# Kernel tuning notes

Measured on AMD Instinct MI355X. Metric: run time of the kernel, lower is better.

## Reference

```python
import jax, jax.numpy as jnp
import numpy as np

N_EMBD = 1024
N_HEAD = 16
HEAD_SIZE = N_EMBD // N_HEAD  # 64


def rotate_half(x):
    x1, x2 = x[..., : x.shape[-1] // 2], x[..., x.shape[-1] // 2 :]
    return jnp.concatenate([-x2, x1], axis=-1)


def rope_cos_sin(T, head_size, dtype):
    inv_freq = 1.0 / (10000.0 ** (jnp.arange(0, head_size, 2, dtype=jnp.float32) / head_size))
    t = jnp.arange(T, dtype=jnp.float32)
    freqs = jnp.outer(t, inv_freq)  # (T, D/2)
    emb = jnp.concatenate([freqs, freqs], axis=-1)  # (T, D)
    return jnp.cos(emb).astype(dtype), jnp.sin(emb).astype(dtype)


def setup_inputs() -> dict:
    key = jax.random.key(0)
    k1, k2, k3, k4 = jax.random.split(key, 4)
    B, T, C = 4, 4096, N_EMBD
    scale = 1.0 / np.sqrt(C)
    return {
        "x": jax.random.normal(k1, (B, T, C), dtype=jnp.float32),
        "sigma0": jnp.zeros((B, N_HEAD, HEAD_SIZE, HEAD_SIZE), dtype=jnp.float32),
        "w_qkv": jax.random.normal(k2, (3 * C, C), dtype=jnp.float32) * scale,
        "w_proj": jax.random.normal(k3, (C, C), dtype=jnp.float32) * scale,
        "eta": jnp.ones((1,), dtype=jnp.float32) * 0.1,
    }


def reference(x, sigma0, w_qkv, w_proj, eta):
    B, T, C = x.shape
    H, D = N_HEAD, HEAD_SIZE
    qkv = x @ w_qkv.T  # (B,T,3C)
    q, k, v = jnp.split(qkv, 3, axis=-1)
    # (B,T,C) -> (B,H,T,D)
    q = q.reshape(B, T, H, D).transpose(0, 2, 1, 3)
    k = k.reshape(B, T, H, D).transpose(0, 2, 1, 3)
    v = v.reshape(B, T, H, D).transpose(0, 2, 1, 3)
    cos, sin = rope_cos_sin(T, D, x.dtype)  # (T,D) broadcast over (B,H,T,D)
    q = q * cos + rotate_half(q) * sin
    k = k * cos + rotate_half(k) * sin
    q = jax.nn.relu(q)
    k = jax.nn.relu(k)
    # sequential Hebbian fast-weight scan over time
    q_t = q.transpose(2, 0, 1, 3)  # (T,B,H,D)
    k_t = k.transpose(2, 0, 1, 3)
    v_t = v.transpose(2, 0, 1, 3)
    eta_s = eta[0]

    def step(sigma, qkv_step):
        qt, kt, vt = qkv_step  # each (B,H,D)
        out_t = jnp.einsum("bhd,bhde->bhe", qt, sigma)  # read BEFORE update
        sigma = sigma + eta_s * jnp.einsum("bhd,bhe->bhde", kt, vt)
        return sigma, out_t

    sigma_final, outs = jax.lax.scan(step, sigma0, (q_t, k_t, v_t))
    # outs: (T,B,H,D) -> (B,T,C)
    out = outs.transpose(1, 0, 2, 3).reshape(B, T, C)
    out = out @ w_proj.T
    return out, sigma_final
```

## Files before the change

### kernel.cpp

```cpp
#include <hip/hip_runtime.h>
#include <hip/hip_bf16.h>
#include <cstdint>
#include <cstddef>

#define B_   4
#define T_   4096
#define C_   1024
#define H_   16
#define NC_  64
#define M_   (B_*T_)
#define N3_  (3*C_)

typedef __attribute__((ext_vector_type(4))) float  f32x4;
typedef __attribute__((ext_vector_type(8))) __bf16 bf16x8;
typedef __attribute__((ext_vector_type(4))) __bf16 bf16x4;
typedef __attribute__((ext_vector_type(8))) unsigned short u16x8;

__device__ __forceinline__ void glds16(void* lds, const void* g) {
  __builtin_amdgcn_global_load_lds((const __attribute__((address_space(1))) void*)g,
                                   (__attribute__((address_space(3))) void*)lds,
                                   16, 0, 0);
}

__global__ __launch_bounds__(256) void cvt_f32_bf16(const float* __restrict__ in,
                                                    __bf16* __restrict__ out, int n4) {
  int i = blockIdx.x * 256 + threadIdx.x;
  if (i >= n4) return;
  float4 v = reinterpret_cast<const float4*>(in)[i];
  bf16x4 o;
  o[0] = (__bf16)v.x; o[1] = (__bf16)v.y; o[2] = (__bf16)v.z; o[3] = (__bf16)v.w;
  reinterpret_cast<bf16x4*>(out)[i] = o;
}

__global__ __launch_bounds__(256) void rope_tab(float2* __restrict__ tab) {
  int gid = blockIdx.x * 256 + threadIdx.x;
  int t = gid >> 5, dp = gid & 31;
  float invf = exp2f(-(float)dp * (13.287712379549449f / 32.0f));
  float ang = (float)t * invf;
  float s, c;
  sincosf(ang, &s, &c);
  tab[gid] = make_float2(c, s);
}

template<int FUSE>
__global__ __launch_bounds__(256) void gemm_bt(const __bf16* __restrict__ A,
                                               const __bf16* __restrict__ Bt,
                                               void* __restrict__ Cout,
                                               const float2* __restrict__ tab,
                                               int M, int N, int K) {
  __shared__ __bf16 sA[128 * 32];
  __shared__ __bf16 sB[128 * 32];
  const int tid  = threadIdx.x;
  const int lane = tid & 63;
  const int wave = tid >> 6;
  const int wr = wave >> 1, wc = wave & 1;
  const int bm = blockIdx.y, bn = blockIdx.x;

  const int srow = wave * 32 + (lane >> 2);
  const int scol = (lane & 3) * 8;
  const __bf16* Ag = A  + (size_t)(bm * 128 + srow) * K + scol;
  const __bf16* Bg = Bt + (size_t)(bn * 128 + srow) * K + scol;
  __bf16* lA0 = sA + wave * 1024 + lane * 8;
  __bf16* lA1 = lA0 + 512;
  __bf16* lB0 = sB + wave * 1024 + lane * 8;
  __bf16* lB1 = lB0 + 512;

  f32x4 acc[4][4];
#pragma unroll
  for (int i = 0; i < 4; i++)
#pragma unroll
    for (int j = 0; j < 4; j++) acc[i][j] = (f32x4)0.0f;

  const int fr = lane & 15;
  const int kb = (lane >> 4) * 8;

  for (int kt = 0; kt < K; kt += 32) {
    __syncthreads();
    glds16(lA0, Ag + kt);
    glds16(lA1, Ag + (size_t)16 * K + kt);
    glds16(lB0, Bg + kt);
    glds16(lB1, Bg + (size_t)16 * K + kt);
    __syncthreads();
    bf16x8 af[4], bfr[4];
#pragma unroll
    for (int i = 0; i < 4; i++)
      af[i] = *(const bf16x8*)(sA + (wr * 64 + i * 16 + fr) * 32 + kb);
#pragma unroll
    for (int j = 0; j < 4; j++)
      bfr[j] = *(const bf16x8*)(sB + (wc * 64 + j * 16 + fr) * 32 + kb);
#pragma unroll
    for (int i = 0; i < 4; i++)
#pragma unroll
      for (int j = 0; j < 4; j++)
        acc[i][j] = __builtin_amdgcn_mfma_f32_16x16x32_bf16(af[i], bfr[j], acc[i][j], 0, 0, 0);
  }

  const int rg = (lane >> 4) * 4;
  if (FUSE == 1 && bn < 16) {
#pragma unroll
    for (int i = 0; i < 4; i++) {
#pragma unroll
      for (int r = 0; r < 4; r++) {
        size_t row = (size_t)bm * 128 + wr * 64 + i * 16 + rg + r;
        int t = (int)(row & (T_ - 1));
#pragma unroll
        for (int j = 0; j < 2; j++) {
          int dp = j * 16 + fr;
          float2 cs = tab[t * 32 + dp];
          float x1 = acc[i][j][r], x2 = acc[i][j + 2][r];
          float o1 = fmaxf(x1 * cs.x - x2 * cs.y, 0.0f);
          float o2 = fmaxf(x2 * cs.x + x1 * cs.y, 0.0f);
          size_t col = (size_t)bn * 128 + wc * 64 + j * 16 + fr;
          ((__bf16*)Cout)[row * N + col]      = (__bf16)o1;
          ((__bf16*)Cout)[row * N + col + 32] = (__bf16)o2;
        }
      }
    }
  } else {
#pragma unroll
    for (int i = 0; i < 4; i++) {
#pragma unroll
      for (int j = 0; j < 4; j++) {
        size_t row = (size_t)bm * 128 + wr * 64 + i * 16 + rg;
        size_t col = (size_t)bn * 128 + wc * 64 + j * 16 + fr;
#pragma unroll
        for (int r = 0; r < 4; r++) {
          if (FUSE == 2) ((float*)Cout)[(row + r) * N + col]  = acc[i][j][r];
          else           ((__bf16*)Cout)[(row + r) * N + col] = (__bf16)acc[i][j][r];
        }
      }
    }
  }
}

#define LDW 72
__global__ __launch_bounds__(256) void chunk_kv(const __bf16* __restrict__ qkv,
                                                __bf16* __restrict__ G) {
  __shared__ __bf16 Kt[64 * LDW];
  __shared__ __bf16 Vt[64 * LDW];
  const int bid = blockIdx.x;
  const int c = bid & (NC_ - 1);
  const int bh = bid >> 6;
  const int h = bh & (H_ - 1);
  const int b = bh >> 4;
  const int tid = threadIdx.x;
  const size_t row0 = (size_t)b * T_ + c * 64;
  const int kcol = C_ + h * 64;
  const int vcol = 2 * C_ + h * 64;
#pragma unroll
  for (int it = 0; it < 2; ++it) {
    int task = tid + it * 256;
    int t = task >> 3;
    int d0 = (task & 7) * 8;
    const size_t rb = (row0 + t) * N3_;
    u16x8 kv = *(const u16x8*)(qkv + rb + kcol + d0);
    u16x8 vv = *(const u16x8*)(qkv + rb + vcol + d0);
#pragma unroll
    for (int j = 0; j < 8; j++) {
      ((unsigned short*)Kt)[(d0 + j) * LDW + t] = kv[j];
      ((unsigned short*)Vt)[(d0 + j) * LDW + t] = vv[j];
    }
  }
  __syncthreads();
  const int lane = tid & 63, wave = tid >> 6;
  const int gr = (wave >> 1) * 32, gc = (wave & 1) * 32;
  const int fr = lane & 15, kb = (lane >> 4) * 8;
  f32x4 acc[2][2];
#pragma unroll
  for (int i = 0; i < 2; i++)
#pragma unroll
    for (int j = 0; j < 2; j++) acc[i][j] = (f32x4)0.0f;
#pragma unroll
  for (int kk = 0; kk < 2; ++kk) {
    bf16x8 af[2], bfr[2];
#pragma unroll
    for (int i = 0; i < 2; i++)
      af[i] = *(const bf16x8*)(Kt + (gr + i * 16 + fr) * LDW + kk * 32 + kb);
#pragma unroll
    for (int j = 0; j < 2; j++)
      bfr[j] = *(const bf16x8*)(Vt + (gc + j * 16 + fr) * LDW + kk * 32 + kb);
#pragma unroll
    for (int i = 0; i < 2; i++)
#pragma unroll
      for (int j = 0; j < 2; j++)
        acc[i][j] = __builtin_amdgcn_mfma_f32_16x16x32_bf16(af[i], bfr[j], acc[i][j], 0, 0, 0);
  }
  const int rg = (lane >> 4) * 4;
  __bf16* Gb = G + (size_t)bid * 4096;
#pragma unroll
  for (int i = 0; i < 2; i++)
#pragma unroll
    for (int j = 0; j < 2; j++)
#pragma unroll
      for (int r = 0; r < 4; r++)
        Gb[(gr + i * 16 + rg + r) * 64 + gc + j * 16 + fr] = (__bf16)acc[i][j][r];
}

__global__ __launch_bounds__(256) void prefix_scan(const __bf16* __restrict__ G,
                                                   const float* __restrict__ sigma0,
                                                   __bf16* __restrict__ S,
                                                   float* __restrict__ sigma_out,
                                                   const float* __restrict__ eta) {
  const int blk = blockIdx.x;
  const int bh = blk >> 2;
  const int dq = blk & 3;
  const int tid = threadIdx.x;
  const int d = dq * 16 + (tid >> 4);
  const int e0 = (tid & 15) * 4;
  const float eta_s = eta[0];
  const size_t base_de = (size_t)d * 64 + e0;
  float acc[4], s0[4];
#pragma unroll
  for (int j = 0; j < 4; j++) {
    acc[j] = 0.0f;
    s0[j] = sigma0[(size_t)bh * 4096 + base_de + j];
  }
  for (int c = 0; c < NC_; ++c) {
    const size_t off = ((size_t)bh * NC_ + c) * 4096 + base_de;
    bf16x4 sv;
#pragma unroll
    for (int j = 0; j < 4; j++) sv[j] = (__bf16)(s0[j] + eta_s * acc[j]);
    *(bf16x4*)(S + off) = sv;
    bf16x4 g = *(const bf16x4*)(G + off);
#pragma unroll
    for (int j = 0; j < 4; j++) acc[j] += (float)g[j];
  }
  float4 v;
  v.x = s0[0] + eta_s * acc[0];
  v.y = s0[1] + eta_s * acc[1];
  v.z = s0[2] + eta_s * acc[2];
  v.w = s0[3] + eta_s * acc[3];
  *reinterpret_cast<float4*>(sigma_out + (size_t)bh * 4096 + base_de) = v;
}

__global__ __launch_bounds__(256) void chunk_out(const __bf16* __restrict__ qkv,
                                                 const __bf16* __restrict__ S,
                                                 __bf16* __restrict__ outp,
                                                 const float* __restrict__ eta) {
  __shared__ __bf16 Qs[64 * LDW];
  __shared__ __bf16 Ks[64 * LDW];
  __shared__ __bf16 Vt[64 * LDW];
  __shared__ __bf16 St[64 * LDW];
  __shared__ __bf16 Ps[64 * LDW];
  const int bid = blockIdx.x;
  const int c = bid & 63, bh = bid >> 6, h = bh & 15, b = bh >> 4;
  const int tid = threadIdx.x;
  const size_t row0 = (size_t)b * T_ + c * 64;
  const float eta_s = eta[0];
#pragma unroll
  for (int it = 0; it < 2; ++it) {
    int task = tid + it * 256;
    int t = task >> 3, d0 = (task & 7) * 8;
    const size_t rb = (row0 + t) * N3_;
    *(u16x8*)(Qs + t * LDW + d0) = *(const u16x8*)(qkv + rb + h * 64 + d0);
    *(u16x8*)(Ks + t * LDW + d0) = *(const u16x8*)(qkv + rb + C_ + h * 64 + d0);
    u16x8 vv = *(const u16x8*)(qkv + rb + 2 * C_ + h * 64 + d0);
    u16x8 sv = *(const u16x8*)(S + (size_t)bid * 4096 + t * 64 + d0);
#pragma unroll
    for (int j = 0; j < 8; j++) {
      ((unsigned short*)Vt)[(d0 + j) * LDW + t] = vv[j];
      ((unsigned short*)St)[(d0 + j) * LDW + t] = sv[j];
    }
  }
  __syncthreads();
  const int lane = tid & 63, wave = tid >> 6;
  const int qr = (wave >> 1) * 32, qc = (wave & 1) * 32;
  const int fr = lane & 15, kb = (lane >> 4) * 8, rg = (lane >> 4) * 4;
  {
    f32x4 pacc[2][2];
#pragma unroll
    for (int i = 0; i < 2; i++)
#pragma unroll
      for (int j = 0; j < 2; j++) pacc[i][j] = (f32x4)0.0f;
#pragma unroll
    for (int kk = 0; kk < 2; ++kk) {
      bf16x8 af[2], bfr[2];
#pragma unroll
      for (int i = 0; i < 2; i++)
        af[i] = *(const bf16x8*)(Qs + (qr + i * 16 + fr) * LDW + kk * 32 + kb);
#pragma unroll
      for (int j = 0; j < 2; j++)
        bfr[j] = *(const bf16x8*)(Ks + (qc + j * 16 + fr) * LDW + kk * 32 + kb);
#pragma unroll
      for (int i = 0; i < 2; i++)
#pragma unroll
        for (int j = 0; j < 2; j++)
          pacc[i][j] = __builtin_amdgcn_mfma_f32_16x16x32_bf16(af[i], bfr[j], pacc[i][j], 0, 0, 0);
    }
#pragma unroll
    for (int i = 0; i < 2; i++)
#pragma unroll
      for (int j = 0; j < 2; j++)
#pragma unroll
        for (int r = 0; r < 4; r++) {
          int trow = qr + i * 16 + rg + r;
          int scol = qc + j * 16 + fr;
          float v = (scol < trow) ? eta_s * pacc[i][j][r] : 0.0f;
          Ps[trow * LDW + scol] = (__bf16)v;
        }
  }
  __syncthreads();
  {
    f32x4 oacc[2][2];
#pragma unroll
    for (int i = 0; i < 2; i++)
#pragma unroll
      for (int j = 0; j < 2; j++) oacc[i][j] = (f32x4)0.0f;
#pragma unroll
    for (int kk = 0; kk < 2; ++kk) {
      bf16x8 pa[2], vb[2], qa[2], sb[2];
#pragma unroll
      for (int i = 0; i < 2; i++) {
        pa[i] = *(const bf16x8*)(Ps + (qr + i * 16 + fr) * LDW + kk * 32 + kb);
        qa[i] = *(const bf16x8*)(Qs + (qr + i * 16 + fr) * LDW + kk * 32 + kb);
      }
#pragma unroll
      for (int j = 0; j < 2; j++) {
        vb[j] = *(const bf16x8*)(Vt + (qc + j * 16 + fr) * LDW + kk * 32 + kb);
        sb[j] = *(const bf16x8*)(St + (qc + j * 16 + fr) * LDW + kk * 32 + kb);
      }
#pragma unroll
      for (int i = 0; i < 2; i++)
#pragma unroll
        for (int j = 0; j < 2; j++) {
          oacc[i][j] = __builtin_amdgcn_mfma_f32_16x16x32_bf16(pa[i], vb[j], oacc[i][j], 0, 0, 0);
          oacc[i][j] = __builtin_amdgcn_mfma_f32_16x16x32_bf16(qa[i], sb[j], oacc[i][j], 0, 0, 0);
        }
    }
#pragma unroll
    for (int i = 0; i < 2; i++)
#pragma unroll
      for (int j = 0; j < 2; j++)
#pragma unroll
        for (int r = 0; r < 4; r++) {
          size_t row = row0 + qr + i * 16 + rg + r;
          int col = h * 64 + qc + j * 16 + fr;
          outp[row * C_ + col] = (__bf16)oacc[i][j][r];
        }
  }
}

extern "C" void kernel_launch(void* const* d_in, const int* in_sizes, int n_in,
                              void* d_out, int out_size, void* d_ws, size_t ws_size,
                              hipStream_t stream) {
  const float* x      = (const float*)d_in[0];
  const float* sigma0 = (const float*)d_in[1];
  const float* w_qkv  = (const float*)d_in[2];
  const float* w_proj = (const float*)d_in[3];
  const float* eta    = (const float*)d_in[4];
  float* out       = (float*)d_out;
  float* sigma_out = out + (size_t)M_ * C_;

  char* ws = (char*)d_ws;
  __bf16* xbf     = (__bf16*)(ws);
  __bf16* wqkvbf  = (__bf16*)(ws + 33554432);
  __bf16* wprojbf = (__bf16*)(ws + 39845888);
  __bf16* qkvbf   = (__bf16*)(ws + 41943040);
  __bf16* Gws     = (__bf16*)(ws + 142606336);
  __bf16* Sws     = (__bf16*)(ws + 176160768);
  float2* tab     = (float2*)(ws + 176160768);

  rope_tab<<<512, 256, 0, stream>>>(tab);
  cvt_f32_bf16<<<16384, 256, 0, stream>>>(x, xbf, 4194304);
  cvt_f32_bf16<<<3072, 256, 0, stream>>>(w_qkv, wqkvbf, 786432);
  cvt_f32_bf16<<<1024, 256, 0, stream>>>(w_proj, wprojbf, 262144);
  gemm_bt<1><<<dim3(24, 128), 256, 0, stream>>>(xbf, wqkvbf, (void*)qkvbf, tab, M_, N3_, C_);
  chunk_kv<<<4096, 256, 0, stream>>>(qkvbf, Gws);
  prefix_scan<<<256, 256, 0, stream>>>(Gws, sigma0, Sws, sigma_out, eta);
  chunk_out<<<4096, 256, 0, stream>>>(qkvbf, Sws, xbf, eta);
  gemm_bt<2><<<dim3(8, 128), 256, 0, stream>>>(xbf, wprojbf, (void*)out, nullptr, M_, C_, C_);
}
```

Measured before the change: 296.6 us.

## Replace QKV GEMM with triple-buffered 256x128 tile pipelined kernel

Result: faster. 280.4 us (-5.5%).

```diff
diff --git a/kernel.cpp b/kernel.cpp
--- a/kernel.cpp
+++ b/kernel.cpp
@@ -10,6 +10,7 @@
 #define NC_  64
 #define M_   (B_*T_)
 #define N3_  (3*C_)
+#define G1_NT 16
 
 typedef __attribute__((ext_vector_type(4))) float  f32x4;
 typedef __attribute__((ext_vector_type(8))) __bf16 bf16x8;
@@ -21,6 +22,7 @@
                                    (__attribute__((address_space(3))) void*)lds,
                                    16, 0, 0);
 }
+#define MFMA_BF16 __builtin_amdgcn_mfma_f32_16x16x32_bf16
 
 __global__ __launch_bounds__(256) void cvt_f32_bf16(const float* __restrict__ in,
                                                     __bf16* __restrict__ out, int n4) {
@@ -42,12 +44,150 @@
   tab[gid] = make_float2(c, s);
 }
 
-template<int FUSE>
-__global__ __launch_bounds__(256) void gemm_bt(const __bf16* __restrict__ A,
-                                               const __bf16* __restrict__ Bt,
-                                               void* __restrict__ Cout,
-                                               const float2* __restrict__ tab,
-                                               int M, int N, int K) {
+__global__ __launch_bounds__(512) void gemm1_pipe(const __bf16* __restrict__ A,
+                                                  const __bf16* __restrict__ Bt,
+                                                  __bf16* __restrict__ Cout,
+                                                  const float2* __restrict__ tab) {
+  __shared__ __bf16 sA[3][256 * 64];
+  __shared__ __bf16 sB[3][128 * 64];
+  const int tid  = threadIdx.x;
+  const int lane = tid & 63;
+  const int wave = tid >> 6;
+  const int wm = wave >> 1, wn = wave & 1;
+  const int bm = blockIdx.y, bn = blockIdx.x;
+  const int fr = lane & 15, kq = lane >> 4;
+  const int fr7 = fr & 7;
+  const int K = C_;
+
+  const int r_loc = tid >> 3;
+  const int sslot = (tid & 7) ^ (r_loc & 7);
+  const __bf16* Ag = A  + (size_t)(bm * 256 + r_loc) * K + sslot * 8;
+  const __bf16* Bg = Bt + (size_t)(bn * 128 + r_loc) * K + sslot * 8;
+
+  f32x4 acc[4][4];
+#pragma unroll
+  for (int i = 0; i < 4; i++)
+#pragma unroll
+    for (int j = 0; j < 4; j++) acc[i][j] = (f32x4)0.0f;
+
+#pragma unroll
+  for (int t = 0; t < 2; ++t) {
+#pragma unroll
+    for (int q = 0; q < 4; ++q)
+      glds16((char*)sA[t] + q * 8192 + tid * 16, Ag + (size_t)q * 64 * K + t * 64);
+#pragma unroll
+    for (int q = 0; q < 2; ++q)
+      glds16((char*)sB[t] + q * 8192 + tid * 16, Bg + (size_t)q * 64 * K + t * 64);
+  }
+  asm volatile("s_waitcnt vmcnt(6)" ::: "memory");
+  __builtin_amdgcn_sched_barrier(0);
+  __builtin_amdgcn_s_barrier();
+
+  bf16x8 af[4][2], bf01[2][2], bf23[2][2];
+  for (int t = 0; t < G1_NT; ++t) {
+    const int buf  = t % 3;
+    const int nbuf = (t + 2) % 3;
+    const bool dostage = (t + 2 < G1_NT);
+    const int kb2 = (t + 2) * 64;
+    const __bf16* Ab = (const __bf16*)sA[buf];
+    const __bf16* Bb = (const __bf16*)sB[buf];
+
+    if (dostage) {
+      glds16((char*)sA[nbuf] +     0 + tid * 16, Ag + (size_t)0 * 64 * K + kb2);
+      glds16((char*)sA[nbuf] +  8192 + tid * 16, Ag + (size_t)1 * 64 * K + kb2);
+      glds16((char*)sA[nbuf] + 16384 + tid * 16, Ag + (size_t)2 * 64 * K + kb2);
+    }
+#pragma unroll
+    for (int i = 0; i < 4; ++i)
+#pragma unroll
+      for (int kk = 0; kk < 2; ++kk)
+        af[i][kk] = *(const bf16x8*)((const char*)Ab + (wm * 64 + i * 16 + fr) * 128 +
+                                     (((kk << 2) | kq) ^ fr7) * 16);
+#pragma unroll
+    for (int j = 0; j < 2; ++j)
+#pragma unroll
+      for (int kk = 0; kk < 2; ++kk)
+        bf01[j][kk] = *(const bf16x8*)((const char*)Bb + (wn * 64 + j * 16 + fr) * 128 +
+                                       (((kk << 2) | kq) ^ fr7) * 16);
+    __builtin_amdgcn_s_barrier();
+    __builtin_amdgcn_s_setprio(1);
+#pragma unroll
+    for (int i = 0; i < 4; ++i)
+#pragma unroll
+      for (int j = 0; j < 2; ++j) {
+        acc[i][j] = MFMA_BF16(af[i][0], bf01[j][0], acc[i][j], 0, 0, 0);
+        acc[i][j] = MFMA_BF16(af[i][1], bf01[j][1], acc[i][j], 0, 0, 0);
+      }
+    __builtin_amdgcn_s_setprio(0);
+    __builtin_amdgcn_s_barrier();
+
+    if (dostage) {
+      glds16((char*)sA[nbuf] + 24576 + tid * 16, Ag + (size_t)3 * 64 * K + kb2);
+      glds16((char*)sB[nbuf] +     0 + tid * 16, Bg + (size_t)0 * 64 * K + kb2);
+      glds16((char*)sB[nbuf] +  8192 + tid * 16, Bg + (size_t)1 * 64 * K + kb2);
+    }
+#pragma unroll
+    for (int j = 0; j < 2; ++j)
+#pragma unroll
+      for (int kk = 0; kk < 2; ++kk)
+        bf23[j][kk] = *(const bf16x8*)((const char*)Bb + (wn * 64 + (j + 2) * 16 + fr) * 128 +
+                                       (((kk << 2) | kq) ^ fr7) * 16);
+    __builtin_amdgcn_s_barrier();
+    __builtin_amdgcn_s_setprio(1);
+#pragma unroll
+    for (int i = 0; i < 4; ++i)
+#pragma unroll
+      for (int j = 0; j < 2; ++j) {
+        acc[i][j + 2] = MFMA_BF16(af[i][0], bf23[j][0], acc[i][j + 2], 0, 0, 0);
+        acc[i][j + 2] = MFMA_BF16(af[i][1], bf23[j][1], acc[i][j + 2], 0, 0, 0);
+      }
+    __builtin_amdgcn_s_setprio(0);
+    if (t < G1_NT - 1) {
+      if (dostage) asm volatile("s_waitcnt vmcnt(6)" ::: "memory");
+      else         asm volatile("s_waitcnt vmcnt(0)" ::: "memory");
+      __builtin_amdgcn_sched_barrier(0);
+    }
+    __builtin_amdgcn_s_barrier();
+  }
+
+  const int rg4 = kq * 4;
+  if (bn < 16) {
+#pragma unroll
+    for (int i = 0; i < 4; ++i)
+#pragma unroll
+      for (int r = 0; r < 4; ++r) {
+        size_t row = (size_t)bm * 256 + wm * 64 + i * 16 + rg4 + r;
+        int tt = (int)(row & (T_ - 1));
+#pragma unroll
+        for (int j = 0; j < 2; ++j) {
+          int dp = j * 16 + fr;
+          float2 cs = tab[tt * 32 + dp];
+          float x1 = acc[i][j][r], x2 = acc[i][j + 2][r];
+          float o1 = fmaxf(x1 * cs.x - x2 * cs.y, 0.0f);
+          float o2 = fmaxf(x2 * cs.x + x1 * cs.y, 0.0f);
+          size_t col = (size_t)bn * 128 + wn * 64 + j * 16 + fr;
+          Cout[row * N3_ + col]      = (__bf16)o1;
+          Cout[row * N3_ + col + 32] = (__bf16)o2;
+        }
+      }
+  } else {
+#pragma unroll
+    for (int i = 0; i < 4; ++i)
+#pragma unroll
+      for (int j = 0; j < 4; ++j) {
+        size_t row = (size_t)bm * 256 + wm * 64 + i * 16 + rg4;
+        size_t col = (size_t)bn * 128 + wn * 64 + j * 16 + fr;
+#pragma unroll
+        for (int r = 0; r < 4; ++r)
+          Cout[(row + r) * N3_ + col] = (__bf16)acc[i][j][r];
+      }
+  }
+}
+
+__global__ __launch_bounds__(256) void gemm_bt_f32(const __bf16* __restrict__ A,
+                                                   const __bf16* __restrict__ Bt,
+                                                   float* __restrict__ Cout,
+                                                   int M, int N, int K) {
   __shared__ __bf16 sA[128 * 32];
   __shared__ __bf16 sB[128 * 32];
   const int tid  = threadIdx.x;
@@ -92,45 +232,20 @@
     for (int i = 0; i < 4; i++)
 #pragma unroll
       for (int j = 0; j < 4; j++)
-        acc[i][j] = __builtin_amdgcn_mfma_f32_16x16x32_bf16(af[i], bfr[j], acc[i][j], 0, 0, 0);
+        acc[i][j] = MFMA_BF16(af[i], bfr[j], acc[i][j], 0, 0, 0);
   }
 
   const int rg = (lane >> 4) * 4;
-  if (FUSE == 1 && bn < 16) {
-#pragma unroll
-    for (int i = 0; i < 4; i++) {
-#pragma unroll
-      for (int r = 0; r < 4; r++) {
-        size_t row = (size_t)bm * 128 + wr * 64 + i * 16 + rg + r;
-        int t = (int)(row & (T_ - 1));
-#pragma unroll
-        for (int j = 0; j < 2; j++) {
-          int dp = j * 16 + fr;
-          float2 cs = tab[t * 32 + dp];
-          float x1 = acc[i][j][r], x2 = acc[i][j + 2][r];
-          float o1 = fmaxf(x1 * cs.x - x2 * cs.y, 0.0f);
-          float o2 = fmaxf(x2 * cs.x + x1 * cs.y, 0.0f);
-          size_t col = (size_t)bn * 128 + wc * 64 + j * 16 + fr;
-          ((__bf16*)Cout)[row * N + col]      = (__bf16)o1;
-          ((__bf16*)Cout)[row * N + col + 32] = (__bf16)o2;
-        }
-      }
-    }
-  } else {
-#pragma unroll
-    for (int i = 0; i < 4; i++) {
-#pragma unroll
-      for (int j = 0; j < 4; j++) {
-        size_t row = (size_t)bm * 128 + wr * 64 + i * 16 + rg;
-        size_t col = (size_t)bn * 128 + wc * 64 + j * 16 + fr;
-#pragma unroll
-        for (int r = 0; r < 4; r++) {
-          if (FUSE == 2) ((float*)Cout)[(row + r) * N + col]  = acc[i][j][r];
-          else           ((__bf16*)Cout)[(row + r) * N + col] = (__bf16)acc[i][j][r];
-        }
-      }
-    }
-  }
+#pragma unroll
+  for (int i = 0; i < 4; i++)
+#pragma unroll
+    for (int j = 0; j < 4; j++) {
+      size_t row = (size_t)bm * 128 + wr * 64 + i * 16 + rg;
+      size_t col = (size_t)bn * 128 + wc * 64 + j * 16 + fr;
+#pragma unroll
+      for (int r = 0; r < 4; r++)
+        Cout[(row + r) * N + col] = acc[i][j][r];
+    }
 }
 
 #define LDW 72
@@ -183,7 +298,7 @@
     for (int i = 0; i < 2; i++)
 #pragma unroll
       for (int j = 0; j < 2; j++)
-        acc[i][j] = __builtin_amdgcn_mfma_f32_16x16x32_bf16(af[i], bfr[j], acc[i][j], 0, 0, 0);
+        acc[i][j] = MFMA_BF16(af[i], bfr[j], acc[i][j], 0, 0, 0);
   }
   const int rg = (lane >> 4) * 4;
   __bf16* Gb = G + (size_t)bid * 4096;
@@ -285,7 +400,7 @@
       for (int i = 0; i < 2; i++)
 #pragma unroll
         for (int j = 0; j < 2; j++)
-          pacc[i][j] = __builtin_amdgcn_mfma_f32_16x16x32_bf16(af[i], bfr[j], pacc[i][j], 0, 0, 0);
+          pacc[i][j] = MFMA_BF16(af[i], bfr[j], pacc[i][j], 0, 0, 0);
     }
 #pragma unroll
     for (int i = 0; i < 2; i++)
@@ -323,8 +438,8 @@
       for (int i = 0; i < 2; i++)
 #pragma unroll
         for (int j = 0; j < 2; j++) {
-          oacc[i][j] = __builtin_amdgcn_mfma_f32_16x16x32_bf16(pa[i], vb[j], oacc[i][j], 0, 0, 0);
-          oacc[i][j] = __builtin_amdgcn_mfma_f32_16x16x32_bf16(qa[i], sb[j], oacc[i][j], 0, 0, 0);
+          oacc[i][j] = MFMA_BF16(pa[i], vb[j], oacc[i][j], 0, 0, 0);
+          oacc[i][j] = MFMA_BF16(qa[i], sb[j], oacc[i][j], 0, 0, 0);
         }
     }
 #pragma unroll
@@ -364,9 +479,9 @@
   cvt_f32_bf16<<<16384, 256, 0, stream>>>(x, xbf, 4194304);
   cvt_f32_bf16<<<3072, 256, 0, stream>>>(w_qkv, wqkvbf, 786432);
   cvt_f32_bf16<<<1024, 256, 0, stream>>>(w_proj, wprojbf, 262144);
-  gemm_bt<1><<<dim3(24, 128), 256, 0, stream>>>(xbf, wqkvbf, (void*)qkvbf, tab, M_, N3_, C_);
+  gemm1_pipe<<<dim3(24, 64), 512, 0, stream>>>(xbf, wqkvbf, qkvbf, tab);
   chunk_kv<<<4096, 256, 0, stream>>>(qkvbf, Gws);
   prefix_scan<<<256, 256, 0, stream>>>(Gws, sigma0, Sws, sigma_out, eta);
   chunk_out<<<4096, 256, 0, stream>>>(qkvbf, Sws, xbf, eta);
-  gemm_bt<2><<<dim3(8, 128), 256, 0, stream>>>(xbf, wprojbf, (void*)out, nullptr, M_, C_, C_);
-}
+  gemm_bt_f32<<<dim3(8, 128), 256, 0, stream>>>(xbf, wprojbf, out, M_, C_, C_);
+}
```

## Replace GEMM with 256x256-tile, 4-stage async LDS pipeline and swizzled layout

Applied to the files above, without the earlier changes.

Result: slower. 310.4 us (+4.7%).

```diff
diff --git a/kernel.cpp b/kernel.cpp
--- a/kernel.cpp
+++ b/kernel.cpp
@@ -10,6 +10,7 @@
 #define NC_  64
 #define M_   (B_*T_)
 #define N3_  (3*C_)
+#define NT2  32
 
 typedef __attribute__((ext_vector_type(4))) float  f32x4;
 typedef __attribute__((ext_vector_type(8))) __bf16 bf16x8;
@@ -21,6 +22,7 @@
                                    (__attribute__((address_space(3))) void*)lds,
                                    16, 0, 0);
 }
+#define MFMA_BF16 __builtin_amdgcn_mfma_f32_16x16x32_bf16
 
 __global__ __launch_bounds__(256) void cvt_f32_bf16(const float* __restrict__ in,
                                                     __bf16* __restrict__ out, int n4) {
@@ -43,93 +45,116 @@
 }
 
 template<int FUSE>
-__global__ __launch_bounds__(256) void gemm_bt(const __bf16* __restrict__ A,
-                                               const __bf16* __restrict__ Bt,
-                                               void* __restrict__ Cout,
-                                               const float2* __restrict__ tab,
-                                               int M, int N, int K) {
-  __shared__ __bf16 sA[128 * 32];
-  __shared__ __bf16 sB[128 * 32];
+__global__ __launch_bounds__(512) void gemm_pipe256(const __bf16* __restrict__ A,
+                                                    const __bf16* __restrict__ Bt,
+                                                    void* __restrict__ Cout,
+                                                    const float2* __restrict__ tab,
+                                                    int N) {
+  __shared__ __bf16 sA[4][256 * 32];
+  __shared__ __bf16 sB[4][256 * 32];
   const int tid  = threadIdx.x;
   const int lane = tid & 63;
   const int wave = tid >> 6;
-  const int wr = wave >> 1, wc = wave & 1;
+  const int wm = wave >> 2, wn = wave & 3;
   const int bm = blockIdx.y, bn = blockIdx.x;
-
-  const int srow = wave * 32 + (lane >> 2);
-  const int scol = (lane & 3) * 8;
-  const __bf16* Ag = A  + (size_t)(bm * 128 + srow) * K + scol;
-  const __bf16* Bg = Bt + (size_t)(bn * 128 + srow) * K + scol;
-  __bf16* lA0 = sA + wave * 1024 + lane * 8;
-  __bf16* lA1 = lA0 + 512;
-  __bf16* lB0 = sB + wave * 1024 + lane * 8;
-  __bf16* lB1 = lB0 + 512;
-
-  f32x4 acc[4][4];
-#pragma unroll
-  for (int i = 0; i < 4; i++)
+  const int fr = lane & 15, kq = lane >> 4;
+  const int K = C_;
+
+  const int r_loc = tid >> 2;
+  const int sslot = (tid & 3) ^ (r_loc & 3);
+  const __bf16* Ag = A  + (size_t)(bm * 256 + r_loc) * K + sslot * 8;
+  const __bf16* Bg = Bt + (size_t)(bn * 256 + r_loc) * K + sslot * 8;
+
+  f32x4 acc[8][4];
+#pragma unroll
+  for (int i = 0; i < 8; i++)
 #pragma unroll
     for (int j = 0; j < 4; j++) acc[i][j] = (f32x4)0.0f;
 
-  const int fr = lane & 15;
-  const int kb = (lane >> 4) * 8;
-
-  for (int kt = 0; kt < K; kt += 32) {
-    __syncthreads();
-    glds16(lA0, Ag + kt);
-    glds16(lA1, Ag + (size_t)16 * K + kt);
-    glds16(lB0, Bg + kt);
-    glds16(lB1, Bg + (size_t)16 * K + kt);
-    __syncthreads();
-    bf16x8 af[4], bfr[4];
-#pragma unroll
-    for (int i = 0; i < 4; i++)
-      af[i] = *(const bf16x8*)(sA + (wr * 64 + i * 16 + fr) * 32 + kb);
-#pragma unroll
-    for (int j = 0; j < 4; j++)
-      bfr[j] = *(const bf16x8*)(sB + (wc * 64 + j * 16 + fr) * 32 + kb);
-#pragma unroll
-    for (int i = 0; i < 4; i++)
-#pragma unroll
-      for (int j = 0; j < 4; j++)
-        acc[i][j] = __builtin_amdgcn_mfma_f32_16x16x32_bf16(af[i], bfr[j], acc[i][j], 0, 0, 0);
-  }
-
-  const int rg = (lane >> 4) * 4;
-  if (FUSE == 1 && bn < 16) {
-#pragma unroll
-    for (int i = 0; i < 4; i++) {
-#pragma unroll
-      for (int r = 0; r < 4; r++) {
-        size_t row = (size_t)bm * 128 + wr * 64 + i * 16 + rg + r;
-        int t = (int)(row & (T_ - 1));
-#pragma unroll
-        for (int j = 0; j < 2; j++) {
+#pragma unroll
+  for (int t = 0; t < 3; ++t) {
+    glds16((char*)sA[t] +    0 + tid * 16, Ag + (size_t)0 * 128 * K + t * 32);
+    glds16((char*)sA[t] + 8192 + tid * 16, Ag + (size_t)1 * 128 * K + t * 32);
+    glds16((char*)sB[t] +    0 + tid * 16, Bg + (size_t)0 * 128 * K + t * 32);
+    glds16((char*)sB[t] + 8192 + tid * 16, Bg + (size_t)1 * 128 * K + t * 32);
+  }
+  asm volatile("s_waitcnt vmcnt(8)" ::: "memory");
+  __builtin_amdgcn_sched_barrier(0);
+  __builtin_amdgcn_s_barrier();
+
+  const int swz = (kq ^ (fr & 3)) * 16;
+  bf16x8 af[8], bf4[4];
+  for (int t = 0; t < NT2; ++t) {
+    const int buf  = t & 3;
+    const int nbuf = (t + 3) & 3;
+    const __bf16* Ab = (const __bf16*)sA[buf];
+    const __bf16* Bb = (const __bf16*)sB[buf];
+
+    if (t + 3 < NT2) {
+      const int kb3 = (t + 3) * 32;
+      glds16((char*)sA[nbuf] +    0 + tid * 16, Ag + (size_t)0 * 128 * K + kb3);
+      glds16((char*)sA[nbuf] + 8192 + tid * 16, Ag + (size_t)1 * 128 * K + kb3);
+      glds16((char*)sB[nbuf] +    0 + tid * 16, Bg + (size_t)0 * 128 * K + kb3);
+      glds16((char*)sB[nbuf] + 8192 + tid * 16, Bg + (size_t)1 * 128 * K + kb3);
+    }
+
+#pragma unroll
+    for (int i = 0; i < 8; ++i)
+      af[i] = *(const bf16x8*)((const char*)Ab + (wm * 128 + i * 16 + fr) * 64 + swz);
+#pragma unroll
+    for (int j = 0; j < 4; ++j)
+      bf4[j] = *(const bf16x8*)((const char*)Bb + (wn * 64 + j * 16 + fr) * 64 + swz);
+
+    __builtin_amdgcn_s_setprio(1);
+#pragma unroll
+    for (int i = 0; i < 8; ++i)
+#pragma unroll
+      for (int j = 0; j < 4; ++j)
+        acc[i][j] = MFMA_BF16(af[i], bf4[j], acc[i][j], 0, 0, 0);
+    __builtin_amdgcn_s_setprio(0);
+
+    if (t < NT2 - 1) {
+      if (t < NT2 - 3)       asm volatile("s_waitcnt vmcnt(8)" ::: "memory");
+      else if (t == NT2 - 3) asm volatile("s_waitcnt vmcnt(4)" ::: "memory");
+      else                   asm volatile("s_waitcnt vmcnt(0)" ::: "memory");
+      __builtin_amdgcn_sched_barrier(0);
+      __builtin_amdgcn_s_barrier();
+    }
+  }
+
+  const int rg4 = kq * 4;
+  const int cb = bn * 256 + wn * 64;
+  if (FUSE == 1 && bn < 8) {
+#pragma unroll
+    for (int i = 0; i < 8; ++i)
+#pragma unroll
+      for (int r = 0; r < 4; ++r) {
+        size_t row = (size_t)bm * 256 + wm * 128 + i * 16 + rg4 + r;
+        int tt = (int)(row & (T_ - 1));
+#pragma unroll
+        for (int j = 0; j < 2; ++j) {
           int dp = j * 16 + fr;
-          float2 cs = tab[t * 32 + dp];
+          float2 cs = tab[tt * 32 + dp];
           float x1 = acc[i][j][r], x2 = acc[i][j + 2][r];
           float o1 = fmaxf(x1 * cs.x - x2 * cs.y, 0.0f);
           float o2 = fmaxf(x2 * cs.x + x1 * cs.y, 0.0f);
-          size_t col = (size_t)bn * 128 + wc * 64 + j * 16 + fr;
-          ((__bf16*)Cout)[row * N + col]      = (__bf16)o1;
-          ((__bf16*)Cout)[row * N + col + 32] = (__bf16)o2;
+          ((__bf16*)Cout)[row * N + cb + j * 16 + fr]      = (__bf16)o1;
+          ((__bf16*)Cout)[row * N + cb + j * 16 + fr + 32] = (__bf16)o2;
         }
       }
-    }
   } else {
 #pragma unroll
-    for (int i = 0; i < 4; i++) {
-#pragma unroll
-      for (int j = 0; j < 4; j++) {
-        size_t row = (size_t)bm * 128 + wr * 64 + i * 16 + rg;
-        size_t col = (size_t)bn * 128 + wc * 64 + j * 16 + fr;
-#pragma unroll
-        for (int r = 0; r < 4; r++) {
+    for (int i = 0; i < 8; ++i)
+#pragma unroll
+      for (int j = 0; j < 4; ++j) {
+        size_t row = (size_t)bm * 256 + wm * 128 + i * 16 + rg4;
+        size_t col = (size_t)cb + j * 16 + fr;
+#pragma unroll
+        for (int r = 0; r < 4; ++r) {
           if (FUSE == 2) ((float*)Cout)[(row + r) * N + col]  = acc[i][j][r];
           else           ((__bf16*)Cout)[(row + r) * N + col] = (__bf16)acc[i][j][r];
         }
       }
-    }
   }
 }
 
@@ -183,7 +208,7 @@
     for (int i = 0; i < 2; i++)
 #pragma unroll
       for (int j = 0; j < 2; j++)
-        acc[i][j] = __builtin_amdgcn_mfma_f32_16x16x32_bf16(af[i], bfr[j], acc[i][j], 0, 0, 0);
+        acc[i][j] = MFMA_BF16(af[i], bfr[j], acc[i][j], 0, 0, 0);
   }
   const int rg = (lane >> 4) * 4;
   __bf16* Gb = G + (size_t)bid * 4096;
@@ -285,7 +310,7 @@
       for (int i = 0; i < 2; i++)
 #pragma unroll
         for (int j = 0; j < 2; j++)
-          pacc[i][j] = __builtin_amdgcn_mfma_f32_16x16x32_bf16(af[i], bfr[j], pacc[i][j], 0, 0, 0);
+          pacc[i][j] = MFMA_BF16(af[i], bfr[j], pacc[i][j], 0, 0, 0);
     }
 #pragma unroll
     for (int i = 0; i < 2; i++)
@@ -323,8 +348,8 @@
       for (int i = 0; i < 2; i++)
 #pragma unroll
         for (int j = 0; j < 2; j++) {
-          oacc[i][j] = __builtin_amdgcn_mfma_f32_16x16x32_bf16(pa[i], vb[j], oacc[i][j], 0, 0, 0);
-          oacc[i][j] = __builtin_amdgcn_mfma_f32_16x16x32_bf16(qa[i], sb[j], oacc[i][j], 0, 0, 0);
+          oacc[i][j] = MFMA_BF16(pa[i], vb[j], oacc[i][j], 0, 0, 0);
+          oacc[i][j] = MFMA_BF16(qa[i], sb[j], oacc[i][j], 0, 0, 0);
         }
     }
 #pragma unroll
@@ -364,9 +389,9 @@
   cvt_f32_bf16<<<16384, 256, 0, stream>>>(x, xbf, 4194304);
   cvt_f32_bf16<<<3072, 256, 0, stream>>>(w_qkv, wqkvbf, 786432);
   cvt_f32_bf16<<<1024, 256, 0, stream>>>(w_proj, wprojbf, 262144);
-  gemm_bt<1><<<dim3(24, 128), 256, 0, stream>>>(xbf, wqkvbf, (void*)qkvbf, tab, M_, N3_, C_);
+  gemm_pipe256<1><<<dim3(12, 64), 512, 0, stream>>>(xbf, wqkvbf, (void*)qkvbf, tab, N3_);
   chunk_kv<<<4096, 256, 0, stream>>>(qkvbf, Gws);
   prefix_scan<<<256, 256, 0, stream>>>(Gws, sigma0, Sws, sigma_out, eta);
   chunk_out<<<4096, 256, 0, stream>>>(qkvbf, Sws, xbf, eta);
-  gemm_bt<2><<<dim3(8, 128), 256, 0, stream>>>(xbf, wprojbf, (void*)out, nullptr, M_, C_, C_);
-}
+  gemm_pipe256<2><<<dim3(4, 64), 512, 0, stream>>>(xbf, wprojbf, (void*)out, nullptr, C_);
+}
```
